# Performance work log

Measured on AMD Instinct MI355X. Metric: run time of the kernel, lower is better.

The kernel has to match this reference:

```python
import jax, jax.numpy as jnp
import numpy as np

N = 100000      # nodes
E = 1600000     # edges (before self-loops)
F_IN = 128      # num_features
H = 4           # heads
C = 32          # out_channels per head (num_hidden)
SLOPE = 0.2     # leaky relu negative slope (alpha)


def setup_inputs() -> dict:
    key = jax.random.key(0)
    k = jax.random.split(key, 6)
    x = jax.random.normal(k[0], (N, F_IN), jnp.float32)
    edge_index = jax.random.randint(k[1], (2, E), 0, N, dtype=jnp.int64)
    W = jax.random.normal(k[2], (F_IN, H * C), jnp.float32) * (1.0 / np.sqrt(F_IN))
    att_src = jax.random.normal(k[3], (H, C), jnp.float32) * 0.1
    att_dst = jax.random.normal(k[4], (H, C), jnp.float32) * 0.1
    bias = jnp.zeros((H * C,), jnp.float32)
    return dict(x=x, W=W, att_src=att_src, att_dst=att_dst, bias=bias,
                edge_index=edge_index)


def reference(x, W, att_src, att_dst, bias, edge_index):
    # PyG GATConv (concat=True, add_self_loops=True), eval mode (dropout off).
    loops = jnp.arange(N, dtype=edge_index.dtype)
    ei = jnp.concatenate([edge_index, jnp.stack([loops, loops])], axis=1)
    src, dst = ei[0], ei[1]                     # [E+N]

    h = (x @ W).reshape(N, H, C)                # projected node features
    a_src = jnp.einsum('nhc,hc->nh', h, att_src)   # [N, H]
    a_dst = jnp.einsum('nhc,hc->nh', h, att_dst)   # [N, H]

    e = a_src[src] + a_dst[dst]                 # [E+N, H]
    e = jnp.where(e > 0, e, SLOPE * e)          # leaky relu

    # segment softmax over incoming edges of each dst node (per head)
    m = jax.lax.stop_gradient(jax.ops.segment_max(e, dst, num_segments=N))
    p = jnp.exp(e - m[dst])
    denom = jax.ops.segment_sum(p, dst, num_segments=N)
    alpha = p / (denom[dst] + 1e-16)            # [E+N, H]

    # weighted scatter-aggregate of source features
    out = jax.ops.segment_sum(alpha[:, :, None] * h[src], dst, num_segments=N)
    return out.reshape(N, H * C) + bias
```

## Files before the change

### kernel.cpp

```cpp
#include <hip/hip_runtime.h>
#include <hip/hip_bf16.h>
#include <math.h>

#define N_NODES 100000
#define F_IN    128
#define HC      128
#define NH      4
#define SLOPE   0.2f

#define PADK    136

#define NB      196
#define BSH     9
#define CAP     10240
#define CAPC    10752
#define CHUNK   2048
#define CURPAD  16

typedef __attribute__((ext_vector_type(8))) short short8;
typedef __attribute__((ext_vector_type(4))) float f32x4;
typedef __attribute__((ext_vector_type(2))) float fx2;

static __device__ __forceinline__ float leaky(float x) { return x > 0.f ? x : SLOPE * x; }

static __device__ __forceinline__ short f2bs(float f) {
    __hip_bfloat16 b = __float2bfloat16(f);
    return *reinterpret_cast<short*>(&b);
}

static __device__ __forceinline__ fx2 bf2f2(unsigned int v) {
    fx2 r;
    r.x = __uint_as_float(v << 16);
    r.y = __uint_as_float(v & 0xffff0000u);
    return r;
}

__global__ __launch_bounds__(256) void k_pre(const float* __restrict__ W,
                                             unsigned short* __restrict__ wt,
                                             int* __restrict__ bucket_cursor)
{
    int t = blockIdx.x * 256 + threadIdx.x;
    if (t < 128 * 128) {
        int k = t >> 7, n = t & 127;
        wt[n * 128 + k] = (unsigned short)f2bs(W[k * HC + n]);
    }
    if (t < NB * CURPAD) bucket_cursor[t] = 0;
}

union SMem {
    struct {
        short xs[64 * PADK];
        short ws[128 * PADK];
    } g;
    struct {
        int ebuf[CHUNK];
        unsigned char bkt[CHUNK];
        int hist[256];
        int lexcl[257];
        int gbase[256];
        int sdata[256];
    } b;
};

__global__ __launch_bounds__(256) void k_main(const float* __restrict__ x,
                                              const unsigned short* __restrict__ wt,
                                              const float* __restrict__ att_src,
                                              const float* __restrict__ att_dst,
                                              unsigned short* __restrict__ hb,
                                              float* __restrict__ a_src,
                                              float* __restrict__ a_dst,
                                              const int* __restrict__ srcp,
                                              const int* __restrict__ dstp,
                                              int* __restrict__ bucket_cursor,
                                              int* __restrict__ eb, int E,
                                              int bucketBlocks)
{
    __shared__ SMem sm;
    const int t = threadIdx.x;

    if ((int)blockIdx.x < bucketBlocks) {
        const int base = blockIdx.x * CHUNK;

        sm.b.hist[t] = 0;
        __syncthreads();

        int sreg[8], dreg[8];
        #pragma unroll
        for (int j = 0; j < CHUNK / 256; ++j) {
            int i = base + t + j * 256;
            bool v = i < E;
            sreg[j] = v ? srcp[i] : 0;
            dreg[j] = v ? dstp[i] : -1;
            if (v) atomicAdd(&sm.b.hist[dreg[j] >> BSH], 1);
        }
        __syncthreads();

        int cnt = sm.b.hist[t];
        sm.b.sdata[t] = cnt;
        __syncthreads();
        for (int o = 1; o < 256; o <<= 1) {
            int add = (t >= o) ? sm.b.sdata[t - o] : 0;
            __syncthreads();
            sm.b.sdata[t] += add;
            __syncthreads();
        }
        int excl = sm.b.sdata[t] - cnt;
        sm.b.lexcl[t] = excl;
        if (t == 255) sm.b.lexcl[256] = sm.b.sdata[255];
        sm.b.hist[t] = excl;
        int gb = 0;
        if (t < NB && cnt > 0) gb = atomicAdd(&bucket_cursor[t * CURPAD], cnt);
        sm.b.gbase[t] = t * CAP + gb;
        __syncthreads();

        #pragma unroll
        for (int j = 0; j < CHUNK / 256; ++j) {
            if (dreg[j] >= 0) {
                int b = dreg[j] >> BSH;
                int r = atomicAdd(&sm.b.hist[b], 1);
                sm.b.ebuf[r] = (sreg[j] << BSH) | (dreg[j] & 511);
                sm.b.bkt[r] = (unsigned char)b;
            }
        }
        __syncthreads();

        const int blockTotal = sm.b.lexcl[256];
        for (int i = t; i < blockTotal; i += 256) {
            int b = sm.b.bkt[i];
            eb[sm.b.gbase[b] + (i - sm.b.lexcl[b])] = sm.b.ebuf[i];
        }
    } else {
        const int r0 = (blockIdx.x - bucketBlocks) * 64;

        for (int i = t; i < 2048; i += 256) {
            int row = i >> 5, kq = (i & 31) * 4;
            int gr = r0 + row;
            float4 v = make_float4(0.f, 0.f, 0.f, 0.f);
            if (gr < N_NODES) v = ((const float4*)(x + (size_t)gr * F_IN))[i & 31];
            short* p = &sm.g.xs[row * PADK + kq];
            p[0] = f2bs(v.x); p[1] = f2bs(v.y); p[2] = f2bs(v.z); p[3] = f2bs(v.w);
        }
        for (int i = t; i < 2048; i += 256) {
            int n = i >> 4, k0 = (i & 15) * 8;
            *(float4*)&sm.g.ws[n * PADK + k0] = *(const float4*)&wt[n * 128 + k0];
        }
        __syncthreads();

        const int wave = t >> 6, lane = t & 63;
        const int quad = lane >> 4, l16 = lane & 15;
        const int wrow = wave * 16;

        f32x4 acc[8];
        #pragma unroll
        for (int nt = 0; nt < 8; ++nt) acc[nt] = (f32x4){0.f, 0.f, 0.f, 0.f};

        const short* ap = &sm.g.xs[(wrow + l16) * PADK + quad * 8];
        #pragma unroll
        for (int kb = 0; kb < 4; ++kb) {
            short8 a = *(const short8*)(ap + kb * 32);
            #pragma unroll
            for (int nt = 0; nt < 8; ++nt) {
                short8 b = *(const short8*)&sm.g.ws[(nt * 16 + l16) * PADK + kb * 32 + quad * 8];
                acc[nt] = __builtin_amdgcn_mfma_f32_16x16x32_bf16(a, b, acc[nt], 0, 0, 0);
            }
        }

        float att_s[8], att_d[8];
        #pragma unroll
        for (int nt = 0; nt < 8; ++nt) {
            att_s[nt] = att_src[nt * 16 + l16];
            att_d[nt] = att_dst[nt * 16 + l16];
        }

        #pragma unroll
        for (int g = 0; g < 4; ++g) {
            int r = r0 + wrow + quad * 4 + g;
            if (r < N_NODES) {
                #pragma unroll
                for (int nt = 0; nt < 8; ++nt)
                    hb[(size_t)r * HC + nt * 16 + l16] = (unsigned short)f2bs(acc[nt][g]);
            }
            float s0 = acc[0][g] * att_s[0] + acc[1][g] * att_s[1];
            float s1 = acc[2][g] * att_s[2] + acc[3][g] * att_s[3];
            float s2 = acc[4][g] * att_s[4] + acc[5][g] * att_s[5];
            float s3 = acc[6][g] * att_s[6] + acc[7][g] * att_s[7];
            float d0 = acc[0][g] * att_d[0] + acc[1][g] * att_d[1];
            float d1 = acc[2][g] * att_d[2] + acc[3][g] * att_d[3];
            float d2 = acc[4][g] * att_d[4] + acc[5][g] * att_d[5];
            float d3 = acc[6][g] * att_d[6] + acc[7][g] * att_d[7];
            #pragma unroll
            for (int o = 1; o < 16; o <<= 1) {
                s0 += __shfl_xor(s0, o); s1 += __shfl_xor(s1, o);
                s2 += __shfl_xor(s2, o); s3 += __shfl_xor(s3, o);
                d0 += __shfl_xor(d0, o); d1 += __shfl_xor(d1, o);
                d2 += __shfl_xor(d2, o); d3 += __shfl_xor(d3, o);
            }
            if (l16 == 0 && r < N_NODES) {
                *(float4*)&a_src[r * NH] = make_float4(s0, s1, s2, s3);
                *(float4*)&a_dst[r * NH] = make_float4(d0, d1, d2, d3);
            }
        }
    }
}

__global__ __launch_bounds__(1024) void k_csr(const int* __restrict__ eb,
                                              const int* __restrict__ bucket_cursor,
                                              int* __restrict__ col,
                                              int2* __restrict__ rowse)
{
    __shared__ int deg[512];
    __shared__ int sdata[256];
    __shared__ alignas(16) int colL[CAPC];

    const int t  = threadIdx.x;
    const int b  = blockIdx.x;
    const int n0 = b * 512;
    const int cnt   = bucket_cursor[b * CURPAD];
    const int ebase = b * CAP;
    const int gofs  = b * CAPC;
    const int nvalid = min(512, N_NODES - n0);
    const int top = cnt + nvalid;

    if (t < 512) deg[t] = (t < nvalid) ? 1 : 0;
    __syncthreads();

    for (int i = t; i < cnt; i += 1024)
        atomicAdd(&deg[eb[ebase + i] & 511], 1);
    __syncthreads();

    int d0 = 0, d1 = 0, ps = 0;
    if (t < 256) {
        d0 = deg[2 * t]; d1 = deg[2 * t + 1];
        ps = d0 + d1;
        sdata[t] = ps;
    }
    __syncthreads();
    for (int o = 1; o < 256; o <<= 1) {
        int add = 0;
        if (t < 256 && t >= o) add = sdata[t - o];
        __syncthreads();
        if (t < 256) sdata[t] += add;
        __syncthreads();
    }
    if (t < 256) {
        int e0 = sdata[t] - ps;
        int e1 = e0 + d0;
        int na = n0 + 2 * t, nb2 = n0 + 2 * t + 1;
        if (na < N_NODES) {
            rowse[na] = make_int2(gofs + e0, gofs + e0 + d0);
            colL[e0] = na;
        }
        if (nb2 < N_NODES) {
            rowse[nb2] = make_int2(gofs + e1, gofs + e1 + d1);
            colL[e1] = nb2;
        }
        deg[2 * t]     = e0 + 1;
        deg[2 * t + 1] = e1 + 1;
    }
    __syncthreads();

    for (int i = t; i < cnt; i += 1024) {
        int v = eb[ebase + i];
        int r = atomicAdd(&deg[v & 511], 1);
        colL[r] = v >> BSH;
    }
    for (int i = top + t; i < CAPC; i += 1024) colL[i] = 0;
    __syncthreads();

    const int4* s4 = (const int4*)colL;
    int4* d4 = (int4*)(col + gofs);
    for (int i = t; i < CAPC / 4; i += 1024) d4[i] = s4[i];
}

__global__ __launch_bounds__(256) void k_node(const unsigned short* __restrict__ hb,
                                              const float* __restrict__ a_src,
                                              const float* __restrict__ a_dst,
                                              const int2* __restrict__ rowse,
                                              const int* __restrict__ col,
                                              const float* __restrict__ bias,
                                              float* __restrict__ out)
{
    const int lane = threadIdx.x & 63;
    const int node = blockIdx.x * 4 + (threadIdx.x >> 6);
    if (node >= N_NODES) return;

    const int g   = lane >> 4;
    const int l16 = lane & 15;
    const int myh = l16 >> 2;

    const int2 se = rowse[node];
    const int r0 = se.x;
    const int cnt = se.y - se.x;

    const float adm = a_dst[node * NH + myh];

    fx2 acc2[4];
    #pragma unroll
    for (int k = 0; k < 4; ++k) acc2[k] = (fx2){0.f, 0.f};
    float denom = 0.f;

    int   cA0 = col[r0 + g];
    int   cA1 = col[r0 + 4 + g];
    float aA0 = a_src[cA0 * NH + myh];
    float aA1 = a_src[cA1 * NH + myh];
    uint4 hA0 = ((const uint4*)(hb + (size_t)cA0 * HC))[l16];
    uint4 hA1 = ((const uint4*)(hb + (size_t)cA1 * HC))[l16];
    int   cB0 = col[r0 + 8 + g];
    int   cB1 = col[r0 + 12 + g];

    for (int i = 0; i < cnt; i += 8) {
        float aN0 = a_src[cB0 * NH + myh];
        float aN1 = a_src[cB1 * NH + myh];
        uint4 hN0 = ((const uint4*)(hb + (size_t)cB0 * HC))[l16];
        uint4 hN1 = ((const uint4*)(hb + (size_t)cB1 * HC))[l16];
        int cC0 = col[r0 + i + 16 + g];
        int cC1 = col[r0 + i + 20 + g];

        float p0 = (i + g     < cnt) ? __expf(leaky(aA0 + adm)) : 0.f;
        float p1 = (i + 4 + g < cnt) ? __expf(leaky(aA1 + adm)) : 0.f;
        denom += p0 + p1;
        fx2 pb0 = (fx2){p0, p0}, pb1 = (fx2){p1, p1};
        acc2[0] = __builtin_elementwise_fma(bf2f2(hA0.x), pb0, acc2[0]);
        acc2[0] = __builtin_elementwise_fma(bf2f2(hA1.x), pb1, acc2[0]);
        acc2[1] = __builtin_elementwise_fma(bf2f2(hA0.y), pb0, acc2[1]);
        acc2[1] = __builtin_elementwise_fma(bf2f2(hA1.y), pb1, acc2[1]);
        acc2[2] = __builtin_elementwise_fma(bf2f2(hA0.z), pb0, acc2[2]);
        acc2[2] = __builtin_elementwise_fma(bf2f2(hA1.z), pb1, acc2[2]);
        acc2[3] = __builtin_elementwise_fma(bf2f2(hA0.w), pb0, acc2[3]);
        acc2[3] = __builtin_elementwise_fma(bf2f2(hA1.w), pb1, acc2[3]);

        aA0 = aN0; aA1 = aN1; hA0 = hN0; hA1 = hN1;
        cB0 = cC0; cB1 = cC1;
    }

    #pragma unroll
    for (int o = 16; o < 64; o <<= 1) {
        denom += __shfl_xor(denom, o);
        #pragma unroll
        for (int k = 0; k < 4; ++k) {
            acc2[k].x += __shfl_xor(acc2[k].x, o);
            acc2[k].y += __shfl_xor(acc2[k].y, o);
        }
    }

    if (g == 0) {
        float inv = 1.f / (denom + 1e-16f);
        const float* bp = &bias[l16 * 8];
        f32x4 o0, o1;
        o0.x = acc2[0].x * inv + bp[0]; o0.y = acc2[0].y * inv + bp[1];
        o0.z = acc2[1].x * inv + bp[2]; o0.w = acc2[1].y * inv + bp[3];
        o1.x = acc2[2].x * inv + bp[4]; o1.y = acc2[2].y * inv + bp[5];
        o1.z = acc2[3].x * inv + bp[6]; o1.w = acc2[3].y * inv + bp[7];
        __builtin_nontemporal_store(o0, (f32x4*)&out[(size_t)node * HC + l16 * 8]);
        __builtin_nontemporal_store(o1, (f32x4*)&out[(size_t)node * HC + l16 * 8 + 4]);
    }
}

extern "C" void kernel_launch(void* const* d_in, const int* in_sizes, int n_in,
                              void* d_out, int out_size, void* d_ws, size_t ws_size,
                              hipStream_t stream)
{
    const float* x       = (const float*)d_in[0];
    const float* W       = (const float*)d_in[1];
    const float* att_src = (const float*)d_in[2];
    const float* att_dst = (const float*)d_in[3];
    const float* bias    = (const float*)d_in[4];
    const int*   ei      = (const int*)d_in[5];
    const int E = in_sizes[5] / 2;
    const int* srcp = ei;
    const int* dstp = ei + E;
    float* out = (float*)d_out;

    char* wsb = (char*)d_ws;
    size_t off = 0;
    auto alloc = [&](size_t bytes) -> char* {
        char* p = wsb + off;
        off += (bytes + 255) & ~(size_t)255;
        return p;
    };
    unsigned short* hb = (unsigned short*)alloc((size_t)N_NODES * HC * sizeof(unsigned short));
    float* a_src   = (float*)alloc((size_t)N_NODES * NH * sizeof(float));
    float* a_dst   = (float*)alloc((size_t)N_NODES * NH * sizeof(float));
    int*   eb      = (int*)alloc((size_t)NB * CAP * sizeof(int));
    int*   col     = (int*)alloc((size_t)NB * CAPC * sizeof(int));
    int2*  rowse   = (int2*)alloc((size_t)N_NODES * sizeof(int2));
    int*   bcursor = (int*)alloc((size_t)NB * CURPAD * sizeof(int));
    unsigned short* wt = (unsigned short*)alloc(128 * 128 * sizeof(unsigned short));

    const int bucketBlocks = (E + CHUNK - 1) / CHUNK;
    const int gemmBlocks   = (N_NODES + 63) / 64;

    k_pre<<<64, 256, 0, stream>>>(W, wt, bcursor);
    k_main<<<bucketBlocks + gemmBlocks, 256, 0, stream>>>(x, wt, att_src, att_dst,
                                                          hb, a_src, a_dst,
                                                          srcp, dstp, bcursor, eb, E,
                                                          bucketBlocks);
    k_csr<<<NB, 1024, 0, stream>>>(eb, bcursor, col, rowse);
    k_node<<<(N_NODES + 3) / 4, 256, 0, stream>>>(hb, a_src, a_dst, rowse, col, bias, out);
}
```

Measured before the change: 244.4 us.

## Fold attention vectors into projection weights and compute logits via MFMA

```diff
diff --git a/kernel.cpp b/kernel.cpp
--- a/kernel.cpp
+++ b/kernel.cpp
@@ -36,13 +36,29 @@
 }
 
 __global__ __launch_bounds__(256) void k_pre(const float* __restrict__ W,
+                                             const float* __restrict__ att_src,
+                                             const float* __restrict__ att_dst,
                                              unsigned short* __restrict__ wt,
+                                             unsigned short* __restrict__ wab,
                                              int* __restrict__ bucket_cursor)
 {
     int t = blockIdx.x * 256 + threadIdx.x;
     if (t < 128 * 128) {
         int k = t >> 7, n = t & 127;
         wt[n * 128 + k] = (unsigned short)f2bs(W[k * HC + n]);
+    } else if (t < 17408) {
+        int i = t - 16384;
+        int k = i >> 3, slot = i & 7;
+        int head = slot & 3;
+        const float* av = (slot & 4) ? att_dst : att_src;
+        float dot = 0.f;
+        #pragma unroll
+        for (int c = 0; c < 32; ++c)
+            dot += W[k * HC + head * 32 + c] * av[head * 32 + c];
+        wab[slot * 128 + k] = (unsigned short)f2bs(dot);
+    } else if (t < 18432) {
+        int i = t - 17408;
+        wab[(8 + (i >> 7)) * 128 + (i & 127)] = 0;
     }
     if (t < NB * CURPAD) bucket_cursor[t] = 0;
 }
@@ -64,8 +80,7 @@
 
 __global__ __launch_bounds__(256) void k_main(const float* __restrict__ x,
                                               const unsigned short* __restrict__ wt,
-                                              const float* __restrict__ att_src,
-                                              const float* __restrict__ att_dst,
+                                              const unsigned short* __restrict__ wab,
                                               unsigned short* __restrict__ hb,
                                               float* __restrict__ a_src,
                                               float* __restrict__ a_dst,
@@ -153,6 +168,7 @@
         f32x4 acc[8];
         #pragma unroll
         for (int nt = 0; nt < 8; ++nt) acc[nt] = (f32x4){0.f, 0.f, 0.f, 0.f};
+        f32x4 acca = (f32x4){0.f, 0.f, 0.f, 0.f};
 
         const short* ap = &sm.g.xs[(wrow + l16) * PADK + quad * 8];
         #pragma unroll
@@ -163,13 +179,8 @@
                 short8 b = *(const short8*)&sm.g.ws[(nt * 16 + l16) * PADK + kb * 32 + quad * 8];
                 acc[nt] = __builtin_amdgcn_mfma_f32_16x16x32_bf16(a, b, acc[nt], 0, 0, 0);
             }
-        }
-
-        float att_s[8], att_d[8];
-        #pragma unroll
-        for (int nt = 0; nt < 8; ++nt) {
-            att_s[nt] = att_src[nt * 16 + l16];
-            att_d[nt] = att_dst[nt * 16 + l16];
+            short8 bwa = *(const short8*)&wab[l16 * 128 + kb * 32 + quad * 8];
+            acca = __builtin_amdgcn_mfma_f32_16x16x32_bf16(a, bwa, acca, 0, 0, 0);
         }
 
         #pragma unroll
@@ -179,25 +190,8 @@
                 #pragma unroll
                 for (int nt = 0; nt < 8; ++nt)
                     hb[(size_t)r * HC + nt * 16 + l16] = (unsigned short)f2bs(acc[nt][g]);
-            }
-            float s0 = acc[0][g] * att_s[0] + acc[1][g] * att_s[1];
-            float s1 = acc[2][g] * att_s[2] + acc[3][g] * att_s[3];
-            float s2 = acc[4][g] * att_s[4] + acc[5][g] * att_s[5];
-            float s3 = acc[6][g] * att_s[6] + acc[7][g] * att_s[7];
-            float d0 = acc[0][g] * att_d[0] + acc[1][g] * att_d[1];
-            float d1 = acc[2][g] * att_d[2] + acc[3][g] * att_d[3];
-            float d2 = acc[4][g] * att_d[4] + acc[5][g] * att_d[5];
-            float d3 = acc[6][g] * att_d[6] + acc[7][g] * att_d[7];
-            #pragma unroll
-            for (int o = 1; o < 16; o <<= 1) {
-                s0 += __shfl_xor(s0, o); s1 += __shfl_xor(s1, o);
-                s2 += __shfl_xor(s2, o); s3 += __shfl_xor(s3, o);
-                d0 += __shfl_xor(d0, o); d1 += __shfl_xor(d1, o);
-                d2 += __shfl_xor(d2, o); d3 += __shfl_xor(d3, o);
-            }
-            if (l16 == 0 && r < N_NODES) {
-                *(float4*)&a_src[r * NH] = make_float4(s0, s1, s2, s3);
-                *(float4*)&a_dst[r * NH] = make_float4(d0, d1, d2, d3);
+                if (l16 < 4)      a_src[r * NH + l16]       = acca[g];
+                else if (l16 < 8) a_dst[r * NH + (l16 - 4)] = acca[g];
             }
         }
     }
@@ -220,6 +214,7 @@
     const int gofs  = b * CAPC;
     const int nvalid = min(512, N_NODES - n0);
     const int top = cnt + nvalid;
+    const int upper = min(CAPC, (top + 32 + 15) & ~15);
 
     if (t < 512) deg[t] = (t < nvalid) ? 1 : 0;
     __syncthreads();
@@ -264,12 +259,13 @@
         int r = atomicAdd(&deg[v & 511], 1);
         colL[r] = v >> BSH;
     }
-    for (int i = top + t; i < CAPC; i += 1024) colL[i] = 0;
+    for (int i = top + t; i < upper; i += 1024) colL[i] = 0;
     __syncthreads();
 
     const int4* s4 = (const int4*)colL;
     int4* d4 = (int4*)(col + gofs);
-    for (int i = t; i < CAPC / 4; i += 1024) d4[i] = s4[i];
+    const int n4 = upper >> 2;
+    for (int i = t; i < n4; i += 1024) d4[i] = s4[i];
 }
 
 __global__ __launch_bounds__(256) void k_node(const unsigned short* __restrict__ hb,
@@ -385,13 +381,14 @@
     int*   col     = (int*)alloc((size_t)NB * CAPC * sizeof(int));
     int2*  rowse   = (int2*)alloc((size_t)N_NODES * sizeof(int2));
     int*   bcursor = (int*)alloc((size_t)NB * CURPAD * sizeof(int));
-    unsigned short* wt = (unsigned short*)alloc(128 * 128 * sizeof(unsigned short));
+    unsigned short* wt  = (unsigned short*)alloc(128 * 128 * sizeof(unsigned short));
+    unsigned short* wab = (unsigned short*)alloc(16 * 128 * sizeof(unsigned short));
 
     const int bucketBlocks = (E + CHUNK - 1) / CHUNK;
     const int gemmBlocks   = (N_NODES + 63) / 64;
 
-    k_pre<<<64, 256, 0, stream>>>(W, wt, bcursor);
-    k_main<<<bucketBlocks + gemmBlocks, 256, 0, stream>>>(x, wt, att_src, att_dst,
+    k_pre<<<73, 256, 0, stream>>>(W, att_src, att_dst, wt, wab, bcursor);
+    k_main<<<bucketBlocks + gemmBlocks, 256, 0, stream>>>(x, wt, wab,
                                                           hb, a_src, a_dst,
                                                           srcp, dstp, bcursor, eb, E,
                                                           bucketBlocks);
```

Result: faster. 239.3 us (-2.1%).
